# Kernel optimization log

Measured on AMD Instinct MI355X. Metric: run time of the kernel, lower is better.

Reference implementation:

```python
import jax, jax.numpy as jnp
import numpy as np

NUM_ITERATIONS = 3


def squash(t, axis=-1):
    sn = jnp.sum(t * t, axis=axis, keepdims=True)
    scale = sn / (1.0 + sn)
    return scale * t / jnp.sqrt(sn)


def setup_inputs() -> dict:
    key = jax.random.key(0)
    k1, k2 = jax.random.split(key)
    B, Cin, R = 64, 8, 800
    NC, O = 128, 16
    x = jax.random.normal(k1, (B, Cin, R), dtype=jnp.float32)
    route_weights = jax.random.normal(k2, (NC, R, Cin, O), dtype=jnp.float32)
    return {"x": x, "route_weights": route_weights}


def reference(x, route_weights):
    # x: [B, Cin, R] -> transpose(1,2) -> [B, R, Cin]
    xt = jnp.transpose(x, (0, 2, 1))
    # priors = x[None,:,:,None,:] @ W[:,None] -> [NC, B, R, 1, O]; we drop the
    # singleton dim and keep [NC, B, R, O] (math identical).
    priors = jnp.einsum('bri,crio->cbro', xt, route_weights)
    logits = jnp.zeros_like(priors)
    outputs = None
    for i in range(NUM_ITERATIONS):
        # original custom softmax over dim=2 (route nodes)
        probs = jax.nn.softmax(logits, axis=2)
        outputs = squash(jnp.sum(probs * priors, axis=2, keepdims=True), axis=-1)  # [NC,B,1,O]
        if i != NUM_ITERATIONS - 1:
            delta = jnp.sum(priors * outputs, axis=-1, keepdims=True)  # [NC,B,R,1]
            logits = logits + delta  # broadcast over O, as in torch
    out = jnp.squeeze(outputs, axis=2)          # [NC, B, O]  (squeeze of [NC,B,1,1,O])
    out = jnp.transpose(out, (1, 0, 2))          # [B, NC, O]  (transpose(0,1))
    out = jnp.transpose(out, (0, 2, 1))          # [B, O, NC]  (final transpose(1,2))
    return out
```

## Files before the change

kernel.cpp:

```cpp
#include <hip/hip_runtime.h>
#include <math.h>

namespace {

constexpr int kB   = 64;
constexpr int kCin = 8;
constexpr int kR   = 800;
constexpr int kNC  = 128;
constexpr int kO   = 16;
constexpr int CT   = 256;
constexpr int MT   = 512;
constexpr int NITER = 3;
constexpr size_t WS_NEEDED =
    (size_t)kNC * kO * kR * kCin * sizeof(unsigned short);

typedef _Float16 half2v __attribute__((ext_vector_type(2)));

__device__ __forceinline__ half2v u2h(unsigned int u) {
  union { unsigned int u; half2v h; } x;
  x.u = u;
  return x.h;
}

__device__ __forceinline__ unsigned short f2h(float f) {
  union { _Float16 h; unsigned short s; } x;
  x.h = (_Float16)f;
  return x.s;
}

__device__ __forceinline__ float dpp_xor1_add(float v) {
  const int o = __builtin_amdgcn_mov_dpp(__float_as_int(v), 0xB1, 0xF, 0xF, true);
  return v + __int_as_float(o);
}
__device__ __forceinline__ float dpp_xor2_add(float v) {
  const int o = __builtin_amdgcn_mov_dpp(__float_as_int(v), 0x4E, 0xF, 0xF, true);
  return v + __int_as_float(o);
}

__global__ __launch_bounds__(CT) void conv_w(const float* __restrict__ W,
                                             unsigned short* __restrict__ Wb) {
  __shared__ float tile[32 * 132];
  const int blk = blockIdx.x;
  const int c  = blk / 25;
  const int rt = blk - c * 25;
  const int r0 = rt * 32;
  const int t  = threadIdx.x;

  const float4* src =
      reinterpret_cast<const float4*>(W + ((size_t)c * kR + r0) * kCin * kO);
  #pragma unroll
  for (int k2 = 0; k2 < 4; ++k2) {
    const int i4  = t + k2 * CT;
    const float4 v = src[i4];
    const int fi = i4 * 4, row = fi >> 7, pos = fi & 127;
    *reinterpret_cast<float4*>(&tile[row * 132 + pos]) = v;
  }
  __syncthreads();

  const int o = t >> 4;
  #pragma unroll
  for (int k2 = 0; k2 < 2; ++k2) {
    const int rl = (t & 15) + 16 * k2;
    unsigned int pk[4];
    #pragma unroll
    for (int q = 0; q < 4; ++q) {
      const unsigned int lo = f2h(tile[rl * 132 + (2 * q + 0) * 16 + o]);
      const unsigned int hi = f2h(tile[rl * 132 + (2 * q + 1) * 16 + o]);
      pk[q] = lo | (hi << 16);
    }
    reinterpret_cast<uint4*>(Wb)[(size_t)(c * kO + o) * kR + (r0 + rl)] =
        make_uint4(pk[0], pk[1], pk[2], pk[3]);
  }
}

__global__ __launch_bounds__(MT, 4) void caps_route(
    const float* __restrict__ x, const unsigned short* __restrict__ Wb,
    float* __restrict__ out) {
  constexpr int RST = 20;
  __shared__ float red[128 * RST];
  __shared__ float red2[8 * RST];
  __shared__ float shs[RST];

  const int t = threadIdx.x;
  const int j   = blockIdx.x;
  const int xcd = j & 7;
  const int kk  = j >> 3;
  const int c   = ((kk >> 6) << 3) + xcd;
  const int b   = kk & 63;

  const float* xb  = x + (size_t)b * kCin * kR;
  const bool  has2 = (t < kR - MT);
  const int   r1   = t, r2 = MT + t;

  float P1[kO], P2[kO];
  #pragma unroll
  for (int o = 0; o < kO; ++o) P2[o] = 0.f;

  const uint4* Wc = reinterpret_cast<const uint4*>(Wb) + (size_t)c * kO * kR;

  {
    half2v xp[4];
    #pragma unroll
    for (int q = 0; q < 4; ++q)
      xp[q] = half2v{(_Float16)xb[(2*q) * kR + r1], (_Float16)xb[(2*q+1) * kR + r1]};
    #pragma unroll
    for (int ob = 0; ob < 2; ++ob) {
      uint4 w[8];
      #pragma unroll
      for (int u = 0; u < 8; ++u) w[u] = Wc[(size_t)(ob * 8 + u) * kR + r1];
      #pragma unroll
      for (int u = 0; u < 8; ++u) {
        float a = __builtin_amdgcn_fdot2(u2h(w[u].x), xp[0], 0.f, false);
        a = __builtin_amdgcn_fdot2(u2h(w[u].y), xp[1], a, false);
        a = __builtin_amdgcn_fdot2(u2h(w[u].z), xp[2], a, false);
        a = __builtin_amdgcn_fdot2(u2h(w[u].w), xp[3], a, false);
        P1[ob * 8 + u] = a;
      }
    }
  }
  if (has2) {
    half2v xp[4];
    #pragma unroll
    for (int q = 0; q < 4; ++q)
      xp[q] = half2v{(_Float16)xb[(2*q) * kR + r2], (_Float16)xb[(2*q+1) * kR + r2]};
    #pragma unroll
    for (int ob = 0; ob < 2; ++ob) {
      uint4 w[8];
      #pragma unroll
      for (int u = 0; u < 8; ++u) w[u] = Wc[(size_t)(ob * 8 + u) * kR + r2];
      #pragma unroll
      for (int u = 0; u < 8; ++u) {
        float a = __builtin_amdgcn_fdot2(u2h(w[u].x), xp[0], 0.f, false);
        a = __builtin_amdgcn_fdot2(u2h(w[u].y), xp[1], a, false);
        a = __builtin_amdgcn_fdot2(u2h(w[u].z), xp[2], a, false);
        a = __builtin_amdgcn_fdot2(u2h(w[u].w), xp[3], a, false);
        P2[ob * 8 + u] = a;
      }
    }
  }

  float l1 = 0.f, l2 = 0.f;
  #pragma unroll
  for (int it = 0; it < NITER; ++it) {
    const float e1 = (it == 0) ? 1.f : __expf(l1);
    const float e2 = has2 ? ((it == 0) ? 1.f : __expf(l2)) : 0.f;

    float sp[kO + 1];
    sp[kO] = e1 + e2;
    #pragma unroll
    for (int o = 0; o < kO; ++o) sp[o] = e1 * P1[o] + e2 * P2[o];

    #pragma unroll
    for (int v = 0; v <= kO; ++v) {
      sp[v] = dpp_xor1_add(sp[v]);
      sp[v] = dpp_xor2_add(sp[v]);
    }
    if ((t & 3) == 0) {
      float* row = &red[(t >> 2) * RST];
      #pragma unroll
      for (int q = 0; q < 4; ++q)
        *reinterpret_cast<float4*>(row + 4 * q) =
            make_float4(sp[4*q], sp[4*q+1], sp[4*q+2], sp[4*q+3]);
      row[16] = sp[16];
    }
    __syncthreads();
    if (t < 136) {
      const int q = t / 17, col = t - q * 17;
      float a = 0.f;
      #pragma unroll
      for (int rr = 0; rr < 16; ++rr) a += red[(rr * 8 + q) * RST + col];
      red2[q * RST + col] = a;
    }
    __syncthreads();
    if (t < 17) {
      float a = 0.f;
      #pragma unroll
      for (int q = 0; q < 8; ++q) a += red2[q * RST + t];
      shs[t] = a;
    }
    __syncthreads();

    const float Zi = 1.f / shs[kO];
    float ss = 0.f;
    #pragma unroll
    for (int o = 0; o < kO; ++o) ss += shs[o] * shs[o];
    const float sn = ss * Zi * Zi;
    const float g  = Zi * sqrtf(sn) / (1.f + sn);

    if (it < NITER - 1) {
      float d1 = 0.f, d2 = 0.f;
      #pragma unroll
      for (int o = 0; o < kO; ++o) { d1 += P1[o] * shs[o]; d2 += P2[o] * shs[o]; }
      l1 += d1 * g;
      if (has2) l2 += d2 * g;
    } else {
      if (t < kO) out[(size_t)b * kO * kNC + t * kNC + c] = shs[t] * g;
    }
  }
}

__global__ __launch_bounds__(MT, 4) void caps_route_f32(
    const float* __restrict__ x, const float* __restrict__ W,
    float* __restrict__ out) {
  constexpr int RST = 20;
  __shared__ float red[128 * RST];
  __shared__ float red2[8 * RST];
  __shared__ float shs[RST];

  const int t   = threadIdx.x;
  const int j   = blockIdx.x;
  const int xcd = j & 7;
  const int kk  = j >> 3;
  const int c   = ((kk >> 6) << 3) + xcd;
  const int b   = kk & 63;

  const float* xb  = x + (size_t)b * kCin * kR;
  const bool  has2 = (t < kR - MT);
  const int   r1   = t, r2 = MT + t;

  float P1[kO], P2[kO];
  #pragma unroll
  for (int o = 0; o < kO; ++o) P2[o] = 0.f;
  {
    float xa[kCin];
    #pragma unroll
    for (int i = 0; i < kCin; ++i) xa[i] = xb[i * kR + r1];
    const float* Wc = W + ((size_t)c * kR + r1) * kCin * kO;
    #pragma unroll
    for (int o = 0; o < kO; ++o) {
      float acc = 0.f;
      #pragma unroll
      for (int i = 0; i < kCin; ++i) acc += xa[i] * Wc[i * kO + o];
      P1[o] = acc;
    }
  }
  if (has2) {
    float xa[kCin];
    #pragma unroll
    for (int i = 0; i < kCin; ++i) xa[i] = xb[i * kR + r2];
    const float* Wc = W + ((size_t)c * kR + r2) * kCin * kO;
    #pragma unroll
    for (int o = 0; o < kO; ++o) {
      float acc = 0.f;
      #pragma unroll
      for (int i = 0; i < kCin; ++i) acc += xa[i] * Wc[i * kO + o];
      P2[o] = acc;
    }
  }

  float l1 = 0.f, l2 = 0.f;
  #pragma unroll
  for (int it = 0; it < NITER; ++it) {
    const float e1 = (it == 0) ? 1.f : __expf(l1);
    const float e2 = has2 ? ((it == 0) ? 1.f : __expf(l2)) : 0.f;
    float sp[kO + 1];
    sp[kO] = e1 + e2;
    #pragma unroll
    for (int o = 0; o < kO; ++o) sp[o] = e1 * P1[o] + e2 * P2[o];
    #pragma unroll
    for (int v = 0; v <= kO; ++v) {
      sp[v] = dpp_xor1_add(sp[v]);
      sp[v] = dpp_xor2_add(sp[v]);
    }
    if ((t & 3) == 0) {
      float* row = &red[(t >> 2) * RST];
      #pragma unroll
      for (int q = 0; q < 4; ++q)
        *reinterpret_cast<float4*>(row + 4 * q) =
            make_float4(sp[4*q], sp[4*q+1], sp[4*q+2], sp[4*q+3]);
      row[16] = sp[16];
    }
    __syncthreads();
    if (t < 136) {
      const int q = t / 17, col = t - q * 17;
      float a = 0.f;
      #pragma unroll
      for (int rr = 0; rr < 16; ++rr) a += red[(rr * 8 + q) * RST + col];
      red2[q * RST + col] = a;
    }
    __syncthreads();
    if (t < 17) {
      float a = 0.f;
      #pragma unroll
      for (int q = 0; q < 8; ++q) a += red2[q * RST + t];
      shs[t] = a;
    }
    __syncthreads();
    const float Zi = 1.f / shs[kO];
    float ss = 0.f;
    #pragma unroll
    for (int o = 0; o < kO; ++o) ss += shs[o] * shs[o];
    const float sn = ss * Zi * Zi;
    const float g  = Zi * sqrtf(sn) / (1.f + sn);
    if (it < NITER - 1) {
      float d1 = 0.f, d2 = 0.f;
      #pragma unroll
      for (int o = 0; o < kO; ++o) { d1 += P1[o] * shs[o]; d2 += P2[o] * shs[o]; }
      l1 += d1 * g;
      if (has2) l2 += d2 * g;
    } else {
      if (t < kO) out[(size_t)b * kO * kNC + t * kNC + c] = shs[t] * g;
    }
  }
}

}

extern "C" void kernel_launch(void* const* d_in, const int* in_sizes, int n_in,
                              void* d_out, int out_size, void* d_ws, size_t ws_size,
                              hipStream_t stream) {
  const float* x = (const float*)d_in[0];
  const float* W = (const float*)d_in[1];
  float* out = (float*)d_out;
  (void)in_sizes; (void)n_in; (void)out_size;

  if (ws_size >= WS_NEEDED) {
    unsigned short* Wb = (unsigned short*)d_ws;
    conv_w<<<dim3(kNC * 25), dim3(CT), 0, stream>>>(W, Wb);
    caps_route<<<dim3(kNC * kB), dim3(MT), 0, stream>>>(x, Wb, out);
  } else {
    caps_route_f32<<<dim3(kNC * kB), dim3(MT), 0, stream>>>(x, W, out);
  }
}
```

Before: 203.6 us.

## Process two batches per block to reuse weight loads and fuse reduction stages

Each block now handles a pair of batch elements for one capsule, so every fp16 weight row is loaded once and used for two sets of priors, halving grid size and weight traffic. Priors are kept as packed fp16 to limit register pressure from the doubled state. The cross-wave reduction replaces the second shared-memory pass and one barrier with DPP lane reductions. The risks are lower occupancy or register spills from four prior arrays, and extra fp16 rounding of priors.

```diff
diff --git a/kernel.cpp b/kernel.cpp
--- a/kernel.cpp
+++ b/kernel.cpp
@@ -36,6 +36,10 @@
   const int o = __builtin_amdgcn_mov_dpp(__float_as_int(v), 0x4E, 0xF, 0xF, true);
   return v + __int_as_float(o);
 }
+__device__ __forceinline__ float dpp_mir8_add(float v) {
+  const int o = __builtin_amdgcn_mov_dpp(__float_as_int(v), 0x141, 0xF, 0xF, true);
+  return v + __int_as_float(o);
+}
 
 __global__ __launch_bounds__(CT) void conv_w(const float* __restrict__ W,
                                              unsigned short* __restrict__ Wb) {
@@ -73,128 +77,166 @@
   }
 }
 
+__device__ __forceinline__ void row_priors(const uint4* __restrict__ Wc,
+                                           const float* __restrict__ xb0,
+                                           const float* __restrict__ xb1,
+                                           int r,
+                                           half2v* __restrict__ Pa,
+                                           half2v* __restrict__ Pb) {
+  half2v xa[4], xc[4];
+  #pragma unroll
+  for (int q = 0; q < 4; ++q) {
+    xa[q] = half2v{(_Float16)xb0[(2*q) * kR + r], (_Float16)xb0[(2*q+1) * kR + r]};
+    xc[q] = half2v{(_Float16)xb1[(2*q) * kR + r], (_Float16)xb1[(2*q+1) * kR + r]};
+  }
+  #pragma unroll
+  for (int ob = 0; ob < 2; ++ob) {
+    uint4 w[8];
+    #pragma unroll
+    for (int u = 0; u < 8; ++u) w[u] = Wc[(size_t)(ob * 8 + u) * kR + r];
+    float pa[8], pb[8];
+    #pragma unroll
+    for (int u = 0; u < 8; ++u) {
+      float a = __builtin_amdgcn_fdot2(u2h(w[u].x), xa[0], 0.f, false);
+      a = __builtin_amdgcn_fdot2(u2h(w[u].y), xa[1], a, false);
+      a = __builtin_amdgcn_fdot2(u2h(w[u].z), xa[2], a, false);
+      a = __builtin_amdgcn_fdot2(u2h(w[u].w), xa[3], a, false);
+      pa[u] = a;
+      float bb = __builtin_amdgcn_fdot2(u2h(w[u].x), xc[0], 0.f, false);
+      bb = __builtin_amdgcn_fdot2(u2h(w[u].y), xc[1], bb, false);
+      bb = __builtin_amdgcn_fdot2(u2h(w[u].z), xc[2], bb, false);
+      bb = __builtin_amdgcn_fdot2(u2h(w[u].w), xc[3], bb, false);
+      pb[u] = bb;
+    }
+    #pragma unroll
+    for (int q = 0; q < 4; ++q) {
+      Pa[ob * 4 + q] = half2v{(_Float16)pa[2*q], (_Float16)pa[2*q+1]};
+      Pb[ob * 4 + q] = half2v{(_Float16)pb[2*q], (_Float16)pb[2*q+1]};
+    }
+  }
+}
+
 __global__ __launch_bounds__(MT, 4) void caps_route(
     const float* __restrict__ x, const unsigned short* __restrict__ Wb,
     float* __restrict__ out) {
   constexpr int RST = 20;
-  __shared__ float red[128 * RST];
-  __shared__ float red2[8 * RST];
-  __shared__ float shs[RST];
+  __shared__ float red[2 * 128 * RST];
+  __shared__ float shs[2 * RST];
 
   const int t = threadIdx.x;
   const int j   = blockIdx.x;
   const int xcd = j & 7;
   const int kk  = j >> 3;
-  const int c   = ((kk >> 6) << 3) + xcd;
-  const int b   = kk & 63;
-
-  const float* xb  = x + (size_t)b * kCin * kR;
+  const int c   = ((kk >> 5) << 3) + xcd;
+  const int bp  = kk & 31;
+  const int b0  = 2 * bp, b1 = b0 + 1;
+
+  const float* xb0 = x + (size_t)b0 * kCin * kR;
+  const float* xb1 = x + (size_t)b1 * kCin * kR;
   const bool  has2 = (t < kR - MT);
   const int   r1   = t, r2 = MT + t;
 
-  float P1[kO], P2[kO];
-  #pragma unroll
-  for (int o = 0; o < kO; ++o) P2[o] = 0.f;
+  half2v P00[8], P01[8], P10[8], P11[8];
+  #pragma unroll
+  for (int q = 0; q < 8; ++q) {
+    P01[q] = half2v{(_Float16)0.f, (_Float16)0.f};
+    P11[q] = half2v{(_Float16)0.f, (_Float16)0.f};
+  }
 
   const uint4* Wc = reinterpret_cast<const uint4*>(Wb) + (size_t)c * kO * kR;
 
-  {
-    half2v xp[4];
-    #pragma unroll
-    for (int q = 0; q < 4; ++q)
-      xp[q] = half2v{(_Float16)xb[(2*q) * kR + r1], (_Float16)xb[(2*q+1) * kR + r1]};
-    #pragma unroll
-    for (int ob = 0; ob < 2; ++ob) {
-      uint4 w[8];
-      #pragma unroll
-      for (int u = 0; u < 8; ++u) w[u] = Wc[(size_t)(ob * 8 + u) * kR + r1];
-      #pragma unroll
-      for (int u = 0; u < 8; ++u) {
-        float a = __builtin_amdgcn_fdot2(u2h(w[u].x), xp[0], 0.f, false);
-        a = __builtin_amdgcn_fdot2(u2h(w[u].y), xp[1], a, false);
-        a = __builtin_amdgcn_fdot2(u2h(w[u].z), xp[2], a, false);
-        a = __builtin_amdgcn_fdot2(u2h(w[u].w), xp[3], a, false);
-        P1[ob * 8 + u] = a;
+  row_priors(Wc, xb0, xb1, r1, P00, P10);
+  if (has2) row_priors(Wc, xb0, xb1, r2, P01, P11);
+
+  float l00 = 0.f, l01 = 0.f, l10 = 0.f, l11 = 0.f;
+  #pragma unroll
+  for (int it = 0; it < NITER; ++it) {
+    const float e00 = (it == 0) ? 1.f : __expf(l00);
+    const float e01 = has2 ? ((it == 0) ? 1.f : __expf(l01)) : 0.f;
+    const float e10 = (it == 0) ? 1.f : __expf(l10);
+    const float e11 = has2 ? ((it == 0) ? 1.f : __expf(l11)) : 0.f;
+
+    float sp0[kO + 1], sp1[kO + 1];
+    sp0[kO] = e00 + e01;
+    sp1[kO] = e10 + e11;
+    #pragma unroll
+    for (int q = 0; q < 8; ++q) {
+      sp0[2*q]   = e00 * (float)P00[q].x + e01 * (float)P01[q].x;
+      sp0[2*q+1] = e00 * (float)P00[q].y + e01 * (float)P01[q].y;
+      sp1[2*q]   = e10 * (float)P10[q].x + e11 * (float)P11[q].x;
+      sp1[2*q+1] = e10 * (float)P10[q].y + e11 * (float)P11[q].y;
+    }
+
+    #pragma unroll
+    for (int v = 0; v <= kO; ++v) { sp0[v] = dpp_xor1_add(sp0[v]); sp1[v] = dpp_xor1_add(sp1[v]); }
+    #pragma unroll
+    for (int v = 0; v <= kO; ++v) { sp0[v] = dpp_xor2_add(sp0[v]); sp1[v] = dpp_xor2_add(sp1[v]); }
+
+    if ((t & 3) == 0) {
+      float* ra = &red[(t >> 2) * RST];
+      float* rb = &red[(128 + (t >> 2)) * RST];
+      #pragma unroll
+      for (int q = 0; q < 4; ++q) {
+        *reinterpret_cast<float4*>(ra + 4 * q) =
+            make_float4(sp0[4*q], sp0[4*q+1], sp0[4*q+2], sp0[4*q+3]);
+        *reinterpret_cast<float4*>(rb + 4 * q) =
+            make_float4(sp1[4*q], sp1[4*q+1], sp1[4*q+2], sp1[4*q+3]);
       }
-    }
-  }
-  if (has2) {
-    half2v xp[4];
-    #pragma unroll
-    for (int q = 0; q < 4; ++q)
-      xp[q] = half2v{(_Float16)xb[(2*q) * kR + r2], (_Float16)xb[(2*q+1) * kR + r2]};
-    #pragma unroll
-    for (int ob = 0; ob < 2; ++ob) {
-      uint4 w[8];
-      #pragma unroll
-      for (int u = 0; u < 8; ++u) w[u] = Wc[(size_t)(ob * 8 + u) * kR + r2];
-      #pragma unroll
-      for (int u = 0; u < 8; ++u) {
-        float a = __builtin_amdgcn_fdot2(u2h(w[u].x), xp[0], 0.f, false);
-        a = __builtin_amdgcn_fdot2(u2h(w[u].y), xp[1], a, false);
-        a = __builtin_amdgcn_fdot2(u2h(w[u].z), xp[2], a, false);
-        a = __builtin_amdgcn_fdot2(u2h(w[u].w), xp[3], a, false);
-        P2[ob * 8 + u] = a;
+      ra[16] = sp0[16];
+      rb[16] = sp1[16];
+    }
+    __syncthreads();
+
+    if (t < 136 || (t >= 256 && t < 392)) {
+      const int bsel = t >> 8;
+      const int tt   = t & 255;
+      const int q    = tt & 7, col = tt >> 3;
+      const float* base = &red[bsel * 128 * RST];
+      float a = 0.f;
+      #pragma unroll
+      for (int rr = 0; rr < 16; ++rr) a += base[(rr * 8 + q) * RST + col];
+      a = dpp_xor1_add(a);
+      a = dpp_xor2_add(a);
+      a = dpp_mir8_add(a);
+      if (q == 0) shs[bsel * RST + col] = a;
+    }
+    __syncthreads();
+
+    const float Z0i = 1.f / shs[kO];
+    const float Z1i = 1.f / shs[RST + kO];
+    float ss0 = 0.f, ss1 = 0.f;
+    #pragma unroll
+    for (int o = 0; o < kO; ++o) {
+      ss0 += shs[o] * shs[o];
+      ss1 += shs[RST + o] * shs[RST + o];
+    }
+    const float sn0 = ss0 * Z0i * Z0i;
+    const float g0  = Z0i * sqrtf(sn0) / (1.f + sn0);
+    const float sn1 = ss1 * Z1i * Z1i;
+    const float g1  = Z1i * sqrtf(sn1) / (1.f + sn1);
+
+    if (it < NITER - 1) {
+      float d00 = 0.f, d01 = 0.f, d10 = 0.f, d11 = 0.f;
+      #pragma unroll
+      for (int q = 0; q < 8; ++q) {
+        const float s0a = shs[2*q], s0b = shs[2*q+1];
+        const float s1a = shs[RST + 2*q], s1b = shs[RST + 2*q+1];
+        d00 += (float)P00[q].x * s0a + (float)P00[q].y * s0b;
+        d01 += (float)P01[q].x * s0a + (float)P01[q].y * s0b;
+        d10 += (float)P10[q].x * s1a + (float)P10[q].y * s1b;
+        d11 += (float)P11[q].x * s1a + (float)P11[q].y * s1b;
       }
-    }
-  }
-
-  float l1 = 0.f, l2 = 0.f;
-  #pragma unroll
-  for (int it = 0; it < NITER; ++it) {
-    const float e1 = (it == 0) ? 1.f : __expf(l1);
-    const float e2 = has2 ? ((it == 0) ? 1.f : __expf(l2)) : 0.f;
-
-    float sp[kO + 1];
-    sp[kO] = e1 + e2;
-    #pragma unroll
-    for (int o = 0; o < kO; ++o) sp[o] = e1 * P1[o] + e2 * P2[o];
-
-    #pragma unroll
-    for (int v = 0; v <= kO; ++v) {
-      sp[v] = dpp_xor1_add(sp[v]);
-      sp[v] = dpp_xor2_add(sp[v]);
-    }
-    if ((t & 3) == 0) {
-      float* row = &red[(t >> 2) * RST];
-      #pragma unroll
-      for (int q = 0; q < 4; ++q)
-        *reinterpret_cast<float4*>(row + 4 * q) =
-            make_float4(sp[4*q], sp[4*q+1], sp[4*q+2], sp[4*q+3]);
-      row[16] = sp[16];
-    }
-    __syncthreads();
-    if (t < 136) {
-      const int q = t / 17, col = t - q * 17;
-      float a = 0.f;
-      #pragma unroll
-      for (int rr = 0; rr < 16; ++rr) a += red[(rr * 8 + q) * RST + col];
-      red2[q * RST + col] = a;
-    }
-    __syncthreads();
-    if (t < 17) {
-      float a = 0.f;
-      #pragma unroll
-      for (int q = 0; q < 8; ++q) a += red2[q * RST + t];
-      shs[t] = a;
-    }
-    __syncthreads();
-
-    const float Zi = 1.f / shs[kO];
-    float ss = 0.f;
-    #pragma unroll
-    for (int o = 0; o < kO; ++o) ss += shs[o] * shs[o];
-    const float sn = ss * Zi * Zi;
-    const float g  = Zi * sqrtf(sn) / (1.f + sn);
-
-    if (it < NITER - 1) {
-      float d1 = 0.f, d2 = 0.f;
-      #pragma unroll
-      for (int o = 0; o < kO; ++o) { d1 += P1[o] * shs[o]; d2 += P2[o] * shs[o]; }
-      l1 += d1 * g;
-      if (has2) l2 += d2 * g;
+      l00 += d00 * g0;
+      if (has2) l01 += d01 * g0;
+      l10 += d10 * g1;
+      if (has2) l11 += d11 * g1;
     } else {
-      if (t < kO) out[(size_t)b * kO * kNC + t * kNC + c] = shs[t] * g;
+      if (t < kO) {
+        out[(size_t)b0 * kO * kNC + t * kNC + c] = shs[t] * g0;
+      } else if (t >= 256 && t < 256 + kO) {
+        const int o = t - 256;
+        out[(size_t)b1 * kO * kNC + o * kNC + c] = shs[RST + o] * g1;
+      }
     }
   }
 }
@@ -317,7 +359,7 @@
   if (ws_size >= WS_NEEDED) {
     unsigned short* Wb = (unsigned short*)d_ws;
     conv_w<<<dim3(kNC * 25), dim3(CT), 0, stream>>>(W, Wb);
-    caps_route<<<dim3(kNC * kB), dim3(MT), 0, stream>>>(x, Wb, out);
+    caps_route<<<dim3(kNC * kB / 2), dim3(MT), 0, stream>>>(x, Wb, out);
   } else {
     caps_route_f32<<<dim3(kNC * kB), dim3(MT), 0, stream>>>(x, W, out);
   }
```

After: 368.4 us. 1.81x slower.
